# Optimization experiments

Hardware: AMD Instinct MI355X
Metric: run time of the kernel (lower is better)

## Reference

```python
import jax, jax.numpy as jnp
import numpy as np

N_SPECIES = 4  # species ids 0..3


def setup_inputs() -> dict:
    key = jax.random.key(0)
    k1, k2, k3, k4 = jax.random.split(key, 4)
    NTA, O, NMAX = 65536, 512, 512
    rho = jax.random.normal(k1, (NTA, O), dtype=jnp.float32)
    # per-species expert Linear(O -> NMAX): weights stacked [S, O, NMAX], bias [S, NMAX]
    W = jax.random.normal(k2, (N_SPECIES, O, NMAX), dtype=jnp.float32) * (1.0 / np.sqrt(O))
    b = jax.random.normal(k3, (N_SPECIES, NMAX), dtype=jnp.float32) * 0.01
    symbols = jax.random.randint(k4, (NTA,), 0, N_SPECIES, dtype=jnp.int32)
    return {"rho": rho, "W": W, "b": b, "symbols": symbols}


def reference(rho, W, b, symbols):
    # Faithful to Gj.forward: coeff[mask] = expert_spe(rho[mask]) for each species.
    # Vectorized form: apply each species' Linear to all atoms (dense GEMM),
    # then select per-atom by species mask. Loop is over the small fixed
    # species set (4), not over data dims.
    NTA = rho.shape[0]
    nmax = W.shape[-1]
    coeff = jnp.zeros((NTA, nmax), dtype=rho.dtype)
    for spe in range(W.shape[0]):
        y = rho @ W[spe] + b[spe]            # [NTA, nmax]
        mask = (symbols == spe)[:, None]      # [NTA, 1]
        coeff = jnp.where(mask, y, coeff)
    return coeff
```

## Files before the change

### kernel.cpp

```cpp
#include <hip/hip_runtime.h>


#define NTA   65536
#define DIM_O 512
#define NMAXD 512
#define NSPE  4
#define BM    128
#define BK    64
#define LDAE  72

typedef __attribute__((ext_vector_type(4))) float  f32x4;
typedef __attribute__((ext_vector_type(8))) short  bf16x8;

__device__ __forceinline__ short f2bf(float f) {
    unsigned u = __builtin_bit_cast(unsigned, f);
    u += 0x7FFFu + ((u >> 16) & 1u);
    return (short)(u >> 16);
}

__global__ void build_lists_kernel(const int* __restrict__ sym,
                                   int* __restrict__ counts,
                                   int* __restrict__ lists) {
    int i = blockIdx.x * 256 + threadIdx.x;
    int s = sym[i];
    int lane = threadIdx.x & 63;
    #pragma unroll
    for (int spe = 0; spe < NSPE; ++spe) {
        unsigned long long m = __ballot(s == spe);
        if (m == 0ull) continue;
        int leader = __ffsll(m) - 1;
        int base = 0;
        if (lane == leader) base = atomicAdd(&counts[spe], __popcll(m));
        base = __shfl(base, leader);
        if (s == spe) {
            int pos = __popcll(m & ((1ull << lane) - 1ull));
            lists[spe * NTA + base + pos] = i;
        }
    }
}

__global__ void pack_w_kernel(const float* __restrict__ W, short* __restrict__ Wp) {
    int idx = blockIdx.x * 256 + threadIdx.x;
    int j  = idx & 7;
    int l  = (idx >> 3) & 63;
    int nb = (idx >> 9) & 31;
    int kb = (idx >> 14) & 15;
    int s  = idx >> 18;
    int k = kb * 32 + (l >> 4) * 8 + j;
    int n = nb * 16 + (l & 15);
    Wp[idx] = f2bf(W[((size_t)s * DIM_O + k) * NMAXD + n]);
}

__global__ __launch_bounds__(512, 2)
void gemm_kernel(const float* __restrict__ rho,
                 const short* __restrict__ Wp,
                 const float* __restrict__ bias,
                 const int*  __restrict__ counts,
                 const int*  __restrict__ lists,
                 float* __restrict__ out)
{
    const int s    = blockIdx.x >> 9;
    const int mb   = blockIdx.x & 511;
    const int cnt  = counts[s];
    const int row0 = mb * BM;
    if (row0 >= cnt) return;
    int rows_here = cnt - row0; if (rows_here > BM) rows_here = BM;

    __shared__ int aidx[BM];
    __shared__ __align__(16) short Abuf[2][BM * LDAE];

    const int tid = threadIdx.x;
    if (tid < BM)
        aidx[tid] = (tid < rows_here) ? lists[s * NTA + row0 + tid] : 0;
    __syncthreads();

    const int  srow  = tid >> 2;
    const int  spart = tid & 3;
    const bool sv    = (srow < rows_here);
    const float* gsrc = rho + (size_t)aidx[srow] * DIM_O + spart * 16;

    const int lane = tid & 63;
    const int w    = tid >> 6;
    const int lrow = lane & 15;
    const int lgr  = lane >> 4;

    f32x4 acc[8][4];
    #pragma unroll
    for (int m = 0; m < 8; ++m)
        #pragma unroll
        for (int n = 0; n < 4; ++n) acc[m][n] = (f32x4)0.0f;

    const short* wbase = Wp + (size_t)s * (16 * 32 * 512) + lane * 8;

    f32x4 st[4];
    if (sv) { const f32x4* p = (const f32x4*)gsrc; st[0]=p[0]; st[1]=p[1]; st[2]=p[2]; st[3]=p[3]; }
    else    { st[0]=st[1]=st[2]=st[3]=(f32x4)0.0f; }
    {
        short* dst = &Abuf[0][srow * LDAE + spart * 16];
        short tmp[16];
        #pragma unroll
        for (int i = 0; i < 4; ++i)
            #pragma unroll
            for (int q = 0; q < 4; ++q) tmp[i*4+q] = f2bf(st[i][q]);
        *(bf16x8*)(dst)     = *(const bf16x8*)&tmp[0];
        *(bf16x8*)(dst + 8) = *(const bf16x8*)&tmp[8];
    }
    __syncthreads();

    for (int kt = 0; kt < 8; ++kt) {
        const int buf = kt & 1;
        if (kt + 1 < 8) {
            if (sv) {
                const f32x4* p = (const f32x4*)(gsrc + (kt + 1) * BK);
                st[0]=p[0]; st[1]=p[1]; st[2]=p[2]; st[3]=p[3];
            } else {
                st[0]=st[1]=st[2]=st[3]=(f32x4)0.0f;
            }
        }
        #pragma unroll
        for (int ks = 0; ks < 2; ++ks) {
            const int kb = kt * 2 + ks;
            bf16x8 bfrag[4];
            #pragma unroll
            for (int nf = 0; nf < 4; ++nf)
                bfrag[nf] = *(const bf16x8*)(wbase + (size_t)(kb * 32 + (w * 4 + nf)) * 512);
            #pragma unroll
            for (int mf = 0; mf < 8; ++mf) {
                const bf16x8 afrag =
                    *(const bf16x8*)&Abuf[buf][(mf * 16 + lrow) * LDAE + ks * 32 + lgr * 8];
                #pragma unroll
                for (int nf = 0; nf < 4; ++nf)
                    acc[mf][nf] = __builtin_amdgcn_mfma_f32_16x16x32_bf16(
                        afrag, bfrag[nf], acc[mf][nf], 0, 0, 0);
            }
        }
        __syncthreads();
        if (kt + 1 < 8) {
            short* dst = &Abuf[buf ^ 1][srow * LDAE + spart * 16];
            short tmp[16];
            #pragma unroll
            for (int i = 0; i < 4; ++i)
                #pragma unroll
                for (int q = 0; q < 4; ++q) tmp[i*4+q] = f2bf(st[i][q]);
            *(bf16x8*)(dst)     = *(const bf16x8*)&tmp[0];
            *(bf16x8*)(dst + 8) = *(const bf16x8*)&tmp[8];
            __syncthreads();
        }
    }

    float bv[4];
    #pragma unroll
    for (int nf = 0; nf < 4; ++nf)
        bv[nf] = bias[s * NMAXD + w * 64 + nf * 16 + lrow];
    #pragma unroll
    for (int mf = 0; mf < 8; ++mf) {
        #pragma unroll
        for (int q = 0; q < 4; ++q) {
            const int r = mf * 16 + lgr * 4 + q;
            if (r < rows_here) {
                float* orow = out + (size_t)aidx[r] * NMAXD + w * 64 + lrow;
                #pragma unroll
                for (int nf = 0; nf < 4; ++nf)
                    orow[nf * 16] = acc[mf][nf][q] + bv[nf];
            }
        }
    }
}

extern "C" void kernel_launch(void* const* d_in, const int* in_sizes, int n_in,
                              void* d_out, int out_size, void* d_ws, size_t ws_size,
                              hipStream_t stream) {
    const float* rho = (const float*)d_in[0];
    const float* W   = (const float*)d_in[1];
    const float* b   = (const float*)d_in[2];
    const int*   sym = (const int*)d_in[3];
    float* out = (float*)d_out;

    int*   counts = (int*)d_ws;
    int*   lists  = (int*)((char*)d_ws + 1024);
    short* Wp     = (short*)((char*)d_ws + 1024 + (size_t)NSPE * NTA * 4);

    hipMemsetAsync(counts, 0, NSPE * sizeof(int), stream);
    build_lists_kernel<<<NTA / 256, 256, 0, stream>>>(sym, counts, lists);
    pack_w_kernel<<<(NSPE * DIM_O * NMAXD) / 256, 256, 0, stream>>>(W, Wp);
    gemm_kernel<<<NSPE * (NTA / BM), 512, 0, stream>>>(rho, Wp, b, counts, lists, out);
}
```

Baseline: 148.6 us.

## Shrink GEMM tile to 64 rows with split N halves and fragment-major LDS layout

Each block now covers 64 gathered rows and one 256-column half of the output, using 256 threads instead of 512. The block index is reordered so species and column half vary fastest, which spreads work across species more evenly. The LDS A buffer is stored in MFMA fragment order in place of the padded row layout, and one barrier per k-step is removed. The smaller tiles give more blocks and higher occupancy, but each rho row is now gathered and converted twice, once per column half.

```diff
diff --git a/kernel.cpp b/kernel.cpp
--- a/kernel.cpp
+++ b/kernel.cpp
@@ -5,9 +5,8 @@
 #define DIM_O 512
 #define NMAXD 512
 #define NSPE  4
-#define BM    128
+#define BM    64
 #define BK    64
-#define LDAE  72
 
 typedef __attribute__((ext_vector_type(4))) float  f32x4;
 typedef __attribute__((ext_vector_type(8))) short  bf16x8;
@@ -51,7 +50,7 @@
     Wp[idx] = f2bf(W[((size_t)s * DIM_O + k) * NMAXD + n]);
 }
 
-__global__ __launch_bounds__(512, 2)
+__global__ __launch_bounds__(256, 4)
 void gemm_kernel(const float* __restrict__ rho,
                  const short* __restrict__ Wp,
                  const float* __restrict__ bias,
@@ -59,63 +58,54 @@
                  const int*  __restrict__ lists,
                  float* __restrict__ out)
 {
-    const int s    = blockIdx.x >> 9;
-    const int mb   = blockIdx.x & 511;
-    const int cnt  = counts[s];
+    const int s   = blockIdx.x & 3;
+    const int ch  = (blockIdx.x >> 2) & 1;
+    const int mb  = blockIdx.x >> 3;
+    const int cnt = counts[s];
     const int row0 = mb * BM;
     if (row0 >= cnt) return;
     int rows_here = cnt - row0; if (rows_here > BM) rows_here = BM;
 
     __shared__ int aidx[BM];
-    __shared__ __align__(16) short Abuf[2][BM * LDAE];
+    __shared__ __align__(16) short Abuf[2][8 * 64 * 8];
 
-    const int tid = threadIdx.x;
-    if (tid < BM)
-        aidx[tid] = (tid < rows_here) ? lists[s * NTA + row0 + tid] : 0;
-    __syncthreads();
-
-    const int  srow  = tid >> 2;
-    const int  spart = tid & 3;
-    const bool sv    = (srow < rows_here);
-    const float* gsrc = rho + (size_t)aidx[srow] * DIM_O + spart * 16;
-
+    const int tid  = threadIdx.x;
     const int lane = tid & 63;
     const int w    = tid >> 6;
     const int lrow = lane & 15;
     const int lgr  = lane >> 4;
 
-    f32x4 acc[8][4];
+    if (tid < BM)
+        aidx[tid] = lists[s * NTA + row0 + ((tid < rows_here) ? tid : 0)];
+    __syncthreads();
+
+    const float* gsrc = rho + (size_t)aidx[lane] * DIM_O + w * 16;
+    const short* wbase = Wp + ((size_t)s * 512 + ch * 16 + w * 4) * 512 + lane * 8;
+
+    f32x4 acc[4][4];
     #pragma unroll
-    for (int m = 0; m < 8; ++m)
+    for (int m = 0; m < 4; ++m)
         #pragma unroll
         for (int n = 0; n < 4; ++n) acc[m][n] = (f32x4)0.0f;
 
-    const short* wbase = Wp + (size_t)s * (16 * 32 * 512) + lane * 8;
-
     f32x4 st[4];
-    if (sv) { const f32x4* p = (const f32x4*)gsrc; st[0]=p[0]; st[1]=p[1]; st[2]=p[2]; st[3]=p[3]; }
-    else    { st[0]=st[1]=st[2]=st[3]=(f32x4)0.0f; }
+    { const f32x4* p = (const f32x4*)gsrc; st[0]=p[0]; st[1]=p[1]; st[2]=p[2]; st[3]=p[3]; }
     {
-        short* dst = &Abuf[0][srow * LDAE + spart * 16];
         short tmp[16];
         #pragma unroll
         for (int i = 0; i < 4; ++i)
             #pragma unroll
             for (int q = 0; q < 4; ++q) tmp[i*4+q] = f2bf(st[i][q]);
-        *(bf16x8*)(dst)     = *(const bf16x8*)&tmp[0];
-        *(bf16x8*)(dst + 8) = *(const bf16x8*)&tmp[8];
+        *(bf16x8*)&Abuf[0][((2*w    )*64 + lane)*8] = *(const bf16x8*)&tmp[0];
+        *(bf16x8*)&Abuf[0][((2*w + 1)*64 + lane)*8] = *(const bf16x8*)&tmp[8];
     }
     __syncthreads();
 
     for (int kt = 0; kt < 8; ++kt) {
         const int buf = kt & 1;
-        if (kt + 1 < 8) {
-            if (sv) {
-                const f32x4* p = (const f32x4*)(gsrc + (kt + 1) * BK);
-                st[0]=p[0]; st[1]=p[1]; st[2]=p[2]; st[3]=p[3];
-            } else {
-                st[0]=st[1]=st[2]=st[3]=(f32x4)0.0f;
-            }
+        if (kt < 7) {
+            const f32x4* p = (const f32x4*)(gsrc + (kt + 1) * BK);
+            st[0]=p[0]; st[1]=p[1]; st[2]=p[2]; st[3]=p[3];
         }
         #pragma unroll
         for (int ks = 0; ks < 2; ++ks) {
@@ -123,27 +113,26 @@
             bf16x8 bfrag[4];
             #pragma unroll
             for (int nf = 0; nf < 4; ++nf)
-                bfrag[nf] = *(const bf16x8*)(wbase + (size_t)(kb * 32 + (w * 4 + nf)) * 512);
+                bfrag[nf] = *(const bf16x8*)(wbase + (size_t)(kb * 32 + nf) * 512);
             #pragma unroll
-            for (int mf = 0; mf < 8; ++mf) {
+            for (int mf = 0; mf < 4; ++mf) {
                 const bf16x8 afrag =
-                    *(const bf16x8*)&Abuf[buf][(mf * 16 + lrow) * LDAE + ks * 32 + lgr * 8];
+                    *(const bf16x8*)&Abuf[buf][((ks*4 + lgr)*64 + mf*16 + lrow)*8];
                 #pragma unroll
                 for (int nf = 0; nf < 4; ++nf)
                     acc[mf][nf] = __builtin_amdgcn_mfma_f32_16x16x32_bf16(
                         afrag, bfrag[nf], acc[mf][nf], 0, 0, 0);
             }
         }
-        __syncthreads();
-        if (kt + 1 < 8) {
-            short* dst = &Abuf[buf ^ 1][srow * LDAE + spart * 16];
+        if (kt < 7) {
             short tmp[16];
             #pragma unroll
             for (int i = 0; i < 4; ++i)
                 #pragma unroll
                 for (int q = 0; q < 4; ++q) tmp[i*4+q] = f2bf(st[i][q]);
-            *(bf16x8*)(dst)     = *(const bf16x8*)&tmp[0];
-            *(bf16x8*)(dst + 8) = *(const bf16x8*)&tmp[8];
+            short* base = Abuf[buf ^ 1];
+            *(bf16x8*)&base[((2*w    )*64 + lane)*8] = *(const bf16x8*)&tmp[0];
+            *(bf16x8*)&base[((2*w + 1)*64 + lane)*8] = *(const bf16x8*)&tmp[8];
             __syncthreads();
         }
     }
@@ -151,14 +140,14 @@
     float bv[4];
     #pragma unroll
     for (int nf = 0; nf < 4; ++nf)
-        bv[nf] = bias[s * NMAXD + w * 64 + nf * 16 + lrow];
+        bv[nf] = bias[s * NMAXD + ch * 256 + w * 64 + nf * 16 + lrow];
     #pragma unroll
-    for (int mf = 0; mf < 8; ++mf) {
+    for (int mf = 0; mf < 4; ++mf) {
         #pragma unroll
         for (int q = 0; q < 4; ++q) {
             const int r = mf * 16 + lgr * 4 + q;
             if (r < rows_here) {
-                float* orow = out + (size_t)aidx[r] * NMAXD + w * 64 + lrow;
+                float* orow = out + (size_t)aidx[r] * NMAXD + ch * 256 + w * 64 + lrow;
                 #pragma unroll
                 for (int nf = 0; nf < 4; ++nf)
                     orow[nf * 16] = acc[mf][nf][q] + bv[nf];
@@ -183,5 +172,5 @@
     hipMemsetAsync(counts, 0, NSPE * sizeof(int), stream);
     build_lists_kernel<<<NTA / 256, 256, 0, stream>>>(sym, counts, lists);
     pack_w_kernel<<<(NSPE * DIM_O * NMAXD) / 256, 256, 0, stream>>>(W, Wp);
-    gemm_kernel<<<NSPE * (NTA / BM), 512, 0, stream>>>(rho, Wp, b, counts, lists, out);
+    gemm_kernel<<<NSPE * 2 * (NTA / BM), 256, 0, stream>>>(rho, Wp, b, counts, lists, out);
 }
```

Measured after the change: 148.9 us. About the same (+0.2%).
